# Kernel optimization log

Measured on AMD Instinct MI355X. Metric: run time of the kernel, lower is better.

Reference implementation:

```python
import jax, jax.numpy as jnp
import numpy as np

K = 20          # hard-coded self.k
NEG_SLOPE = 0.01


def _conv_bn_act(x, W, g, b):
    """1x1 conv (W: [Cout,Cin]) + eval-mode BN folded into per-channel g,b + LeakyReLU.
    x: (B, Cin, ...) -> (B, Cout, ...)"""
    y = jnp.einsum('oc,bc...->bo...', W, x)
    shp = (1, -1) + (1,) * (y.ndim - 2)
    return jax.nn.leaky_relu(y * g.reshape(shp) + b.reshape(shp), NEG_SLOPE)


def _knn_idx(x, k):
    """x: (B, C, N) -> idx (B, N, k) of k nearest neighbors (incl. self)."""
    xx = jnp.sum(x * x, axis=1)                      # (B, N)
    inner = jnp.einsum('bcn,bcm->bnm', x, x)         # (B, N, N)
    pair = 2.0 * inner - xx[:, :, None] - xx[:, None, :]  # -||xi-xj||^2
    return jax.lax.top_k(pair, k)[1]


def _gather(xt, idx):
    """xt: (B, N, C), idx: (B, N, k) -> (B, N, k, C)"""
    b = jnp.arange(xt.shape[0])[:, None, None]
    return xt[b, idx]


def _forward(x, w1, g1, b1, w2, g2, b2, wdg1, gdg1, bdg1, wdg2, gdg2, bdg2,
             wsn1, gsn1, bsn1, wsn2, gsn2, bsn2, w3, g3, b3, w4, g4, b4, w5, g5, b5):
    x0 = jnp.transpose(x, (0, 2, 1))                 # (B, 3, N) == xInit3d (t3d=False)
    h = _conv_bn_act(x0, w1, g1, b1)                 # (B, 64, N)
    h = _conv_bn_act(h, w2, g2, b2)                  # (B, 64, N)

    # Dynamic-graph EdgeConv: knn on features, edge = [x_i, x_j - x_i]
    idx1 = _knn_idx(h, K)                            # (B, N, K)
    ht = jnp.transpose(h, (0, 2, 1))                 # (B, N, 64)
    nbr = _gather(ht, idx1)                          # (B, N, K, 64)
    ctr = ht[:, :, None, :]                          # (B, N, 1, 64)
    edge = jnp.concatenate([jnp.broadcast_to(ctr, nbr.shape), nbr - ctr], axis=-1)
    edge = jnp.transpose(edge, (0, 3, 1, 2))         # (B, 128, N, K)
    h = _conv_bn_act(edge, wdg1, gdg1, bdg1)         # (B, 64, N, K)
    h = _conv_bn_act(h, wdg2, gdg2, bdg2)
    h = jnp.max(h, axis=-1)                          # (B, 64, N)

    # Spatial-neighborhood conv: knn on 3D coords, gather features only (cat=False)
    idx2 = _knn_idx(x0, K)                           # (B, N, K)
    feat2 = _gather(jnp.transpose(h, (0, 2, 1)), idx2)   # (B, N, K, 64)
    feat2 = jnp.transpose(feat2, (0, 3, 1, 2))       # (B, 64, N, K)
    h = _conv_bn_act(feat2, wsn1, gsn1, bsn1)
    h = _conv_bn_act(h, wsn2, gsn2, bsn2)
    h = jnp.max(h, axis=-1)                          # (B, 64, N)

    h = _conv_bn_act(h, w3, g3, b3)                  # (B, 64, N)
    h = _conv_bn_act(h, w4, g4, b4)                  # (B, 128, N)
    h = _conv_bn_act(h, w5, g5, b5)                  # (B, 512, N)
    return h[..., None]                             # (B, 512, N, 1)


def setup_inputs() -> dict:
    key = jax.random.key(0)
    ks = jax.random.split(key, 32)
    B, N = 8, 4096
    emb = 512
    d = {"x": jax.random.normal(ks[0], (B, N, 3), dtype=jnp.float32)}
    layers = [("1", 64, 3), ("2", 64, 64), ("dg1", 64, 128), ("dg2", 64, 64),
              ("sn1", 64, 64), ("sn2", 64, 64), ("3", 64, 64), ("4", 128, 64), ("5", emb, 128)]
    i = 1
    for name, co, ci in layers:
        d["w" + name] = jax.random.normal(ks[i], (co, ci), dtype=jnp.float32) * (1.0 / np.sqrt(ci))
        d["g" + name] = 1.0 + 0.1 * jax.random.normal(ks[i + 1], (co,), dtype=jnp.float32)
        d["b" + name] = 0.1 * jax.random.normal(ks[i + 2], (co,), dtype=jnp.float32)
        i += 3
    return d


def reference(x, w1, g1, b1, w2, g2, b2, wdg1, gdg1, bdg1, wdg2, gdg2, bdg2,
              wsn1, gsn1, bsn1, wsn2, gsn2, bsn2, w3, g3, b3, w4, g4, b4, w5, g5, b5):
    return _forward(x, w1, g1, b1, w2, g2, b2, wdg1, gdg1, bdg1, wdg2, gdg2, bdg2,
                    wsn1, gsn1, bsn1, wsn2, gsn2, bsn2, w3, g3, b3, w4, g4, b4, w5, g5, b5)
```

## Files before the change

kernel.cpp:

```cpp
#include <hip/hip_runtime.h>
#include <hip/hip_bf16.h>
#include <stdint.h>

typedef __hip_bfloat16 bf16;

#define N_   4096
#define NP   32768
#define KNN  20

#define OFF_H2   0L
#define OFF_XYZ  2097152L
#define OFF_X    2097152L
#define OFF_Y    2129920L
#define OFF_Z    2162688L
#define OFF_XX   2195456L
#define OFF_XXC  2228224L
#define OFF_IDX1 2260992L
#define OFF_P4   2260992L
#define OFF_IDX2 2916352L
#define OFF_WF   3571712L
#define OFF_FLAG 3676480L
#define OFF_PAIR 3676544L
#define OFF_U    3676544L
#define OFF_V    5773696L
#define OFF_HDG  7870848L
#define OFF_H4   5773696L

#define WF_W1 0
#define WF_G1 192
#define WF_B1 256
#define WF_W2 320
#define WF_G2 4416
#define WF_B2 4480
#define WF_WDG1 4544
#define WF_GDG1 12736
#define WF_BDG1 12800
#define WF_WDG2 12864
#define WF_GDG2 16960
#define WF_BDG2 17024
#define WF_WSN1 17088
#define WF_GSN1 21184
#define WF_BSN1 21248
#define WF_WSN2 21312
#define WF_GSN2 25408
#define WF_BSN2 25472
#define WF_W3 25536
#define WF_G3 29632
#define WF_B3 29696
#define WF_W4 29760
#define WF_G4 37952
#define WF_B4 38080
#define WF_W5 38208
#define WF_G5 103744
#define WF_B5 104256
#define WF_END 104768

__device__ __forceinline__ float lrelu(float x){ return x >= 0.f ? x : 0.01f*x; }

__device__ __forceinline__ float distf(float xn,float yn,float zn,
                                       float xm,float ym,float zm,float cm){
  return fmaf(2.f, fmaf(xn,xm, fmaf(yn,ym, zn*zm)), -cm);
}

template<int CTRL>
__device__ __forceinline__ float fmax_dpp(float v){
  int o = __builtin_amdgcn_update_dpp(0, __float_as_int(v), CTRL, 0xF, 0xF, true);
  return fmaxf(v, __int_as_float(o));
}
__device__ __forceinline__ float wave_max_bcast(float v){
  v = fmax_dpp<0xB1>(v);
  v = fmax_dpp<0x4E>(v);
  v = fmax_dpp<0x124>(v);
  v = fmax_dpp<0x128>(v);
  v = fmax_dpp<0x142>(v);
  v = fmax_dpp<0x143>(v);
  return __int_as_float(__builtin_amdgcn_readlane(__float_as_int(v), 63));
}

__device__ __forceinline__ void ins2(float c, int m, float& k1, int& i1,
                                     float& k2, int& i2){
  bool g1 = c > k1, g2 = c > k2;
  k2 = g2 ? (g1 ? k1 : c) : k2;
  i2 = g2 ? (g1 ? i1 : m) : i2;
  k1 = g1 ? c : k1;
  i1 = g1 ? m : i1;
}

template<int MODE, typename F>
__device__ __forceinline__ void topk_pairs(float k1, int i1, float k2, int i2,
                                           int lane, F&& refetch,
                                           int* __restrict__ outp){
  const float NEGINF = -__builtin_inff();
  uint32_t mlo = 0, mhi = 0;
  int keep = 0;
  #pragma unroll 1
  for (int tt = 0; tt < KNN; tt++){
    float g = wave_max_bcast(k1);
    uint64_t ball = __ballot(k1 == g);
    int js = __builtin_amdgcn_readfirstlane((int)(__ffsll((unsigned long long)ball) - 1));
    int wid = __builtin_amdgcn_readlane(i1, js);
    int kown = __builtin_amdgcn_readlane(__float_as_int(k2), js);
    if (lane == tt) keep = wid;
    bool own = (lane == js);
    uint32_t ord = (MODE == 0) ? ((uint32_t)wid >> 6)
                               : ((((uint32_t)wid >> 8) << 2) | ((uint32_t)wid & 3u));
    uint32_t blo = (ord < 32u) ? (1u << ord) : 0u;
    uint32_t bhi = (ord >= 32u) ? (1u << (ord - 32u)) : 0u;
    mlo |= own ? blo : 0u;
    mhi |= own ? bhi : 0u;
    k1 = own ? k2 : k1;  i1 = own ? i2 : i1;
    k2 = own ? NEGINF : k2;
    if (kown == (int)0xFF800000u){
      uint32_t mre = (MODE == 0)
        ? ((uint32_t)js + ((uint32_t)lane << 6))
        : ((((uint32_t)lane >> 2) << 8) | (((uint32_t)js) << 2) | ((uint32_t)lane & 3u));
      float v = refetch(mre);
      uint32_t bl = (uint32_t)__builtin_amdgcn_readlane((int)mlo, js);
      uint32_t bh = (uint32_t)__builtin_amdgcn_readlane((int)mhi, js);
      uint64_t bm = ((uint64_t)bh << 32) | bl;
      if ((bm >> lane) & 1ull) v = NEGINF;
      float g2 = wave_max_bcast(v);
      uint64_t b2 = __ballot(v == g2);
      int jw = (int)(__ffsll((unsigned long long)b2) - 1);
      uint32_t wm = (MODE == 0)
        ? ((uint32_t)js + ((uint32_t)jw << 6))
        : ((((uint32_t)jw >> 2) << 8) | (((uint32_t)js) << 2) | ((uint32_t)jw & 3u));
      if (lane == js){ k1 = g2; i1 = (int)wm; }
    }
  }
  if (lane < KNN) outp[lane] = keep;
}

__global__ void k_detect(const void* __restrict__ x, int* __restrict__ flag){
  int lane = threadIdx.x;
  const bf16* xb = (const bf16*)x;
  int cnt = 0;
  #pragma unroll 1
  for (int i = lane; i < 256; i += 64){
    float v = __bfloat162float(xb[2*i]);
    float a = fabsf(v);
    if (a > 1e-3f && a < 100.f) cnt++;
  }
  #pragma unroll
  for (int off = 32; off; off >>= 1) cnt += __shfl_down(cnt, off, 64);
  if (lane == 0) *flag = (cnt >= 128) ? 0 : 1;
}

struct WPack {
  const void* p[27];
  int off[28];
};

__global__ void k_wcvt(WPack pk, float* __restrict__ dst, const int* __restrict__ flagp){
  int i = blockIdx.x*256 + threadIdx.x;
  if (i >= WF_END) return;
  int f = *flagp;
  #pragma unroll 1
  for (int s = 0; s < 27; s++){
    if (i < pk.off[s+1]){
      int j = i - pk.off[s];
      dst[i] = f ? ((const float*)pk.p[s])[j]
                 : __bfloat162float(((const bf16*)pk.p[s])[j]);
      return;
    }
  }
}

__global__ void k_point(const void* __restrict__ x, float* __restrict__ ws){
  const float* wf = ws + OFF_WF;
  int f = ((const int*)(ws + OFF_FLAG))[0];
  int n = blockIdx.x*256 + threadIdx.x;
  float x0, x1, x2;
  if (f){
    const float* xf = (const float*)x;
    x0 = xf[n*3+0]; x1 = xf[n*3+1]; x2 = xf[n*3+2];
  } else {
    const bf16* xb = (const bf16*)x;
    x0 = __bfloat162float(xb[n*3+0]);
    x1 = __bfloat162float(xb[n*3+1]);
    x2 = __bfloat162float(xb[n*3+2]);
  }

  float h1[64];
  #pragma unroll
  for (int o=0;o<64;o++){
    float a = wf[WF_W1+o*3+0]*x0 + wf[WF_W1+o*3+1]*x1 + wf[WF_W1+o*3+2]*x2;
    h1[o] = lrelu(wf[WF_G1+o]*a + wf[WF_B1+o]);
  }
  float xx = 0.f;
  #pragma unroll 1
  for (int o=0;o<64;o++){
    float a = 0.f;
    #pragma unroll
    for (int c=0;c<64;c++) a += wf[WF_W2+o*64+c]*h1[c];
    float h2 = lrelu(wf[WF_G2+o]*a + wf[WF_B2+o]);
    ws[OFF_H2 + (long)n*64 + o] = h2;
    xx += h2*h2;
  }
  ws[OFF_XX + n] = xx;
  float cc = x0*x0 + x1*x1 + x2*x2;
  ws[OFF_X + n] = x0; ws[OFF_Y + n] = x1; ws[OFF_Z + n] = x2;
  ws[OFF_XXC + n] = cc;
  *(float4*)(ws + OFF_P4 + 4L*n) = make_float4(x0, x1, x2, cc);
}

__global__ __launch_bounds__(256) void k_pair(const float* __restrict__ ws, float* __restrict__ pair,
                                              int b, int n0){
  __shared__ float As[64*128];
  __shared__ float Bs[64*128];
  int t = threadIdx.x;
  int bx = blockIdx.x, by = blockIdx.y;
  const float* h2 = ws + OFF_H2 + (long)b*N_*64;

  int r = t >> 1, c0 = (t & 1)*32;
  const float4* arow = (const float4*)(h2 + (long)(n0 + by*128 + r)*64 + c0);
  const float4* brow = (const float4*)(h2 + (long)(bx*128 + r)*64 + c0);
  #pragma unroll
  for (int q=0;q<8;q++){
    float4 av = arow[q];
    As[(c0+4*q+0)*128 + r] = av.x; As[(c0+4*q+1)*128 + r] = av.y;
    As[(c0+4*q+2)*128 + r] = av.z; As[(c0+4*q+3)*128 + r] = av.w;
    float4 bv = brow[q];
    Bs[(c0+4*q+0)*128 + r] = bv.x; Bs[(c0+4*q+1)*128 + r] = bv.y;
    Bs[(c0+4*q+2)*128 + r] = bv.z; Bs[(c0+4*q+3)*128 + r] = bv.w;
  }
  __syncthreads();

  int tr = t/16, tc = t%16;
  float acc[8][8] = {};
  #pragma unroll 4
  for (int k=0;k<64;k++){
    const float4* ap = (const float4*)&As[k*128 + tr*8];
    const float4* bp = (const float4*)&Bs[k*128 + tc*8];
    float4 a0 = ap[0], a1 = ap[1], c0v = bp[0], c1v = bp[1];
    float a[8] = {a0.x,a0.y,a0.z,a0.w,a1.x,a1.y,a1.z,a1.w};
    float c[8] = {c0v.x,c0v.y,c0v.z,c0v.w,c1v.x,c1v.y,c1v.z,c1v.w};
    #pragma unroll
    for (int i=0;i<8;i++)
      #pragma unroll
      for (int j=0;j<8;j++) acc[i][j] += a[i]*c[j];
  }
  const float* xxp = ws + OFF_XX + b*N_ + bx*128 + tc*8;
  float xxm[8];
  #pragma unroll
  for (int j=0;j<8;j++) xxm[j] = xxp[j];
  #pragma unroll
  for (int i=0;i<8;i++){
    long row = (long)(by*128 + tr*8 + i)*N_ + bx*128 + tc*8;
    float4 o0 = make_float4(2.f*acc[i][0]-xxm[0], 2.f*acc[i][1]-xxm[1],
                            2.f*acc[i][2]-xxm[2], 2.f*acc[i][3]-xxm[3]);
    float4 o1 = make_float4(2.f*acc[i][4]-xxm[4], 2.f*acc[i][5]-xxm[5],
                            2.f*acc[i][6]-xxm[6], 2.f*acc[i][7]-xxm[7]);
    ((float4*)(pair+row))[0] = o0;
    ((float4*)(pair+row))[1] = o1;
  }
}

__global__ __launch_bounds__(256) void k_topk_pair(const float* __restrict__ pair, int* __restrict__ idx1,
                                                   int b, int n0){
  int t = threadIdx.x;
  int lane = t & 63, wv = t >> 6;
  int r = blockIdx.x*4 + wv;
  const float* rowp = pair + (long)r*N_;
  const float4* src = (const float4*)rowp;
  float k1 = -__builtin_inff(), k2 = -__builtin_inff();
  int i1 = 0, i2 = 0;
  #pragma unroll
  for (int q=0;q<16;q++){
    float4 v = src[lane + 64*q];
    int m0 = 4*lane + 256*q;
    ins2(v.x, m0,   k1,i1,k2,i2);
    ins2(v.y, m0+1, k1,i1,k2,i2);
    ins2(v.z, m0+2, k1,i1,k2,i2);
    ins2(v.w, m0+3, k1,i1,k2,i2);
  }
  topk_pairs<1>(k1,i1,k2,i2, lane, [&](uint32_t mre){ return rowp[mre]; },
                idx1 + (long)(b*N_ + n0 + r)*KNN);
}

__global__ __launch_bounds__(512) void k_knn2(const float* __restrict__ ws, int* __restrict__ idx2){
  __shared__ float4 pbuf[2][512];
  int t = threadIdx.x;
  int lane = t & 63, wv = t >> 6;
  int n = blockIdx.x*8 + wv;
  int base = n & ~4095;
  const float4* P4 = (const float4*)(ws + OFF_P4);
  float4 qp = P4[n];
  float xn = qp.x, yn = qp.y, zn = qp.z;
  float k1 = -__builtin_inff(), k2 = -__builtin_inff();
  int i1 = 0, i2 = 0;

  pbuf[0][t] = P4[base + t];
  __syncthreads();
  #pragma unroll 1
  for (int c = 0; c < 8; c++){
    float4 nx;
    if (c < 7) nx = P4[base + (c+1)*512 + t];
    const float4* pb = pbuf[c & 1];
    #pragma unroll
    for (int j = 0; j < 8; j++){
      float4 p = pb[lane + 64*j];
      int m = c*512 + 64*j + lane;
      ins2(distf(xn,yn,zn, p.x,p.y,p.z,p.w), m, k1,i1,k2,i2);
    }
    __syncthreads();
    if (c < 7) pbuf[(c+1) & 1][t] = nx;
    __syncthreads();
  }
  topk_pairs<0>(k1,i1,k2,i2, lane, [&](uint32_t mre){
      float4 p = P4[base + (int)mre];
      return distf(xn,yn,zn, p.x, p.y, p.z, p.w);
    }, idx2 + (long)n*KNN);
}

__global__ __launch_bounds__(256) void k_uv(float* __restrict__ ws){
  const float* wf = ws + OFF_WF;
  int t = threadIdx.x;
  int lane = t & 63;
  int W = blockIdx.x*4 + (t >> 6);
  int g = __builtin_amdgcn_readfirstlane(W >> 3);
  int s = __builtin_amdgcn_readfirstlane(W & 7);
  int n = g*64 + lane;
  int o0 = s*8;
  float h[64];
  const float4* src = (const float4*)(ws + OFF_H2 + (long)n*64);
  #pragma unroll
  for (int q=0;q<16;q++){ float4 v = src[q]; h[4*q]=v.x; h[4*q+1]=v.y; h[4*q+2]=v.z; h[4*q+3]=v.w; }
  float ua[8], vv[8];
  #pragma unroll 1
  for (int j=0;j<8;j++){
    int o = o0 + j;
    float va=0.f, vb=0.f;
    #pragma unroll
    for (int c=0;c<64;c++){
      va += wf[WF_WDG1+o*128+c]*h[c];
      vb += wf[WF_WDG1+o*128+64+c]*h[c];
    }
    ua[j] = va - vb;
    vv[j] = vb;
  }
  float* up = ws + OFF_U + (long)n*64 + o0;
  *(float4*)up     = make_float4(ua[0],ua[1],ua[2],ua[3]);
  *(float4*)(up+4) = make_float4(ua[4],ua[5],ua[6],ua[7]);
  float* vp = ws + OFF_V + (long)n*64 + o0;
  *(float4*)vp     = make_float4(vv[0],vv[1],vv[2],vv[3]);
  *(float4*)(vp+4) = make_float4(vv[4],vv[5],vv[6],vv[7]);
}

template<int USE_U>
__global__ __launch_bounds__(512) void k_edge(float* __restrict__ ws, const int* __restrict__ idxt,
      long uoff, long goff, int w2off,
      int g1off, int b1off, int g2off, int b2off, long outoff){
  __shared__ float y1t[64*66];
  __shared__ float w2t[64*68];
  __shared__ int   idxs[64*KNN];
  const float* wf = ws + OFF_WF;
  int t = threadIdx.x;
  int p0 = blockIdx.x*64;
  int b  = p0 >> 12;
  int lane = t & 63, wv = t >> 6;
  int tr = t & 31, oc = t >> 5;

  #pragma unroll 1
  for (int i=t;i<4096;i+=512){ int o = i>>6, kk = i&63; w2t[kk*68+o] = wf[w2off + i]; }
  #pragma unroll 1
  for (int i=t;i<64*KNN;i+=512) idxs[i] = idxt[(long)p0*KNN + i];

  float ur[8];
  if (USE_U){
    #pragma unroll
    for (int jj=0;jj<8;jj++)
      ur[jj] = ws[uoff + (long)(p0 + wv*8 + jj)*64 + lane];
  } else {
    #pragma unroll
    for (int jj=0;jj<8;jj++) ur[jj] = 0.f;
  }
  float g1v = wf[g1off+lane], b1v = wf[b1off+lane];
  float g2r[4], b2r[4];
  #pragma unroll
  for (int j=0;j<4;j++){ g2r[j] = wf[g2off+oc*4+j]; b2r[j] = wf[b2off+oc*4+j]; }

  float mx[2][4];
  #pragma unroll
  for (int i=0;i<2;i++)
    #pragma unroll
    for (int j=0;j<4;j++) mx[i][j] = -3.0e38f;

  __syncthreads();

  long gbase = goff + ((long)b << 12)*64;
  float pf[8];
  #pragma unroll
  for (int jj=0;jj<8;jj++){
    int nb = idxs[(wv*8 + jj)*KNN];
    pf[jj] = ws[gbase + (long)nb*64 + lane];
  }

  for (int k=0;k<KNN;k++){
    #pragma unroll
    for (int jj=0;jj<8;jj++){
      int e = wv*8 + jj;
      float val = pf[jj];
      if (USE_U) val += ur[jj];
      y1t[lane*66 + e] = lrelu(g1v*val + b1v);
    }
    __syncthreads();
    if (k+1 < KNN){
      #pragma unroll
      for (int jj=0;jj<8;jj++){
        int nb = idxs[(wv*8 + jj)*KNN + k+1];
        pf[jj] = ws[gbase + (long)nb*64 + lane];
      }
    }
    float acc[2][4] = {};
    #pragma unroll 4
    for (int kk=0;kk<64;kk++){
      float2 a = *(const float2*)&y1t[kk*66 + tr*2];
      float4 c = *(const float4*)&w2t[kk*68 + oc*4];
      float av[2] = {a.x, a.y};
      float cv[4] = {c.x, c.y, c.z, c.w};
      #pragma unroll
      for (int i=0;i<2;i++)
        #pragma unroll
        for (int j=0;j<4;j++) acc[i][j] += av[i]*cv[j];
    }
    #pragma unroll
    for (int i=0;i<2;i++)
      #pragma unroll
      for (int j=0;j<4;j++){
        float yy = lrelu(g2r[j]*acc[i][j] + b2r[j]);
        mx[i][j] = fmaxf(mx[i][j], yy);
      }
    __syncthreads();
  }
  #pragma unroll
  for (int i=0;i<2;i++)
    #pragma unroll
    for (int j=0;j<4;j++)
      ws[outoff + (long)(p0 + tr*2 + i)*64 + oc*4 + j] = mx[i][j];
}

__global__ __launch_bounds__(256) void k_w(float* __restrict__ ws){
  const float* wf = ws + OFF_WF;
  int t = threadIdx.x;
  int lane = t & 63;
  int W = blockIdx.x*4 + (t >> 6);
  int g = __builtin_amdgcn_readfirstlane(W >> 3);
  int s = __builtin_amdgcn_readfirstlane(W & 7);
  int n = g*64 + lane;
  int o0 = s*8;
  float h[64];
  const float4* src = (const float4*)(ws + OFF_HDG + (long)n*64);
  #pragma unroll
  for (int q=0;q<16;q++){ float4 v = src[q]; h[4*q]=v.x; h[4*q+1]=v.y; h[4*q+2]=v.z; h[4*q+3]=v.w; }
  float ua[8];
  #pragma unroll 1
  for (int j=0;j<8;j++){
    int o = o0 + j;
    float a = 0.f;
    #pragma unroll
    for (int c=0;c<64;c++) a += wf[WF_WSN1 + o*64 + c]*h[c];
    ua[j] = a;
  }
  float* up = ws + OFF_U + (long)n*64 + o0;
  *(float4*)up     = make_float4(ua[0],ua[1],ua[2],ua[3]);
  *(float4*)(up+4) = make_float4(ua[4],ua[5],ua[6],ua[7]);
}

__global__ __launch_bounds__(256) void k_h4(const float* __restrict__ ws, float* __restrict__ h4g){
  __shared__ float Hs[64*65];
  __shared__ float wb[64*130];
  const float* wf = ws + OFF_WF;
  int t = threadIdx.x;
  int p0 = blockIdx.x*64;

  {
    int r = t >> 2, c0 = (t & 3)*16;
    const float4* src = (const float4*)(ws + OFF_H2 + (long)(p0 + r)*64 + c0);
    #pragma unroll
    for (int q=0;q<4;q++){
      float4 v = src[q];
      Hs[(c0+4*q+0)*65 + r] = v.x; Hs[(c0+4*q+1)*65 + r] = v.y;
      Hs[(c0+4*q+2)*65 + r] = v.z; Hs[(c0+4*q+3)*65 + r] = v.w;
    }
  }
  {
    int r = t >> 2, c0 = (t & 3)*16;
    const float4* src = (const float4*)(wf + WF_W3 + (long)r*64 + c0);
    #pragma unroll
    for (int q=0;q<4;q++){
      float4 v = src[q];
      wb[(c0+4*q+0)*65 + r] = v.x; wb[(c0+4*q+1)*65 + r] = v.y;
      wb[(c0+4*q+2)*65 + r] = v.z; wb[(c0+4*q+3)*65 + r] = v.w;
    }
  }
  __syncthreads();

  int pr = t & 15, og = t >> 4;
  float acc[4][4] = {};
  #pragma unroll 8
  for (int k=0;k<64;k++){
    float4 a = *(const float4*)&Hs[k*65 + pr*4];
    float4 c = *(const float4*)&wb[k*65 + og*4];
    float av[4] = {a.x,a.y,a.z,a.w}, cv[4] = {c.x,c.y,c.z,c.w};
    #pragma unroll
    for (int i=0;i<4;i++)
      #pragma unroll
      for (int j=0;j<4;j++) acc[i][j] += av[i]*cv[j];
  }
  __syncthreads();

  #pragma unroll
  for (int j=0;j<4;j++){
    int o = og*4 + j;
    float g3 = wf[WF_G3+o], b3 = wf[WF_B3+o];
    #pragma unroll
    for (int i=0;i<4;i++)
      Hs[o*65 + pr*4 + i] = lrelu(g3*acc[i][j] + b3);
  }
  {
    int r = t >> 1, c0 = (t & 1)*32;
    const float4* src = (const float4*)(wf + WF_W4 + (long)r*64 + c0);
    #pragma unroll
    for (int q=0;q<8;q++){
      float4 v = src[q];
      wb[(c0+4*q+0)*130 + r] = v.x; wb[(c0+4*q+1)*130 + r] = v.y;
      wb[(c0+4*q+2)*130 + r] = v.z; wb[(c0+4*q+3)*130 + r] = v.w;
    }
  }
  __syncthreads();

  float a2[4][8] = {};
  #pragma unroll 8
  for (int k=0;k<64;k++){
    float4 a = *(const float4*)&Hs[k*65 + pr*4];
    float4 c0 = *(const float4*)&wb[k*130 + og*8];
    float4 c1 = *(const float4*)&wb[k*130 + og*8 + 4];
    float av[4] = {a.x,a.y,a.z,a.w};
    float cv[8] = {c0.x,c0.y,c0.z,c0.w,c1.x,c1.y,c1.z,c1.w};
    #pragma unroll
    for (int i=0;i<4;i++)
      #pragma unroll
      for (int j=0;j<8;j++) a2[i][j] += av[i]*cv[j];
  }
  #pragma unroll
  for (int j=0;j<8;j++){
    int o = og*8 + j;
    float g4 = wf[WF_G4+o], b4 = wf[WF_B4+o];
    #pragma unroll
    for (int i=0;i<4;i++)
      h4g[(long)o*NP + p0 + pr*4 + i] = lrelu(g4*a2[i][j] + b4);
  }
}

#define KC 32
__global__ __launch_bounds__(256) void k_conv5(const float* __restrict__ ws, void* __restrict__ outv){
  __shared__ float As[KC*128];
  __shared__ float Bs[KC*128];
  const float* wf = ws + OFF_WF;
  int f = ((const int*)(ws + OFF_FLAG))[0];
  int t = threadIdx.x;
  int p0 = blockIdx.x*128;
  int o0 = blockIdx.y*128;
  const float* H4 = ws + OFF_H4;
  float acc[8][8] = {};

  for (int kc = 0; kc < 128; kc += KC){
    {
      int r = t >> 1, c0 = (t & 1)*16;
      const float4* src = (const float4*)(wf + WF_W5 + (long)(o0 + r)*128 + kc + c0);
      #pragma unroll
      for (int q=0;q<4;q++){
        float4 v = src[q];
        As[(c0+4*q+0)*128 + r] = v.x; As[(c0+4*q+1)*128 + r] = v.y;
        As[(c0+4*q+2)*128 + r] = v.z; As[(c0+4*q+3)*128 + r] = v.w;
      }
    }
    {
      int kr = t >> 3, pc = (t & 7)*16;
      const float4* src = (const float4*)(H4 + (long)(kc + kr)*NP + p0 + pc);
      float4 v0 = src[0], v1 = src[1], v2 = src[2], v3 = src[3];
      *(float4*)&Bs[kr*128 + pc     ] = v0;
      *(float4*)&Bs[kr*128 + pc + 4 ] = v1;
      *(float4*)&Bs[kr*128 + pc + 8 ] = v2;
      *(float4*)&Bs[kr*128 + pc + 12] = v3;
    }
    __syncthreads();
    int tr = t/16, tc = t%16;
    #pragma unroll 8
    for (int k=0;k<KC;k++){
      const float4* ap = (const float4*)&As[k*128 + tr*8];
      const float4* bp = (const float4*)&Bs[k*128 + tc*8];
      float4 a0 = ap[0], a1 = ap[1], b0 = bp[0], b1 = bp[1];
      float a[8] = {a0.x,a0.y,a0.z,a0.w,a1.x,a1.y,a1.z,a1.w};
      float b[8] = {b0.x,b0.y,b0.z,b0.w,b1.x,b1.y,b1.z,b1.w};
      #pragma unroll
      for (int i=0;i<8;i++)
        #pragma unroll
        for (int j=0;j<8;j++) acc[i][j] += a[i]*b[j];
    }
    __syncthreads();
  }

  int tr = t/16, tc = t%16;
  int b = p0 >> 12, nn = (p0 & 4095) + tc*8;
  #pragma unroll
  for (int i=0;i<8;i++){
    int oo = o0 + tr*8 + i;
    float g5 = wf[WF_G5+oo], b5 = wf[WF_B5+oo];
    long base = ((long)(b*512 + oo) << 12) + nn;
    if (f){
      float4 v0 = make_float4(lrelu(g5*acc[i][0]+b5), lrelu(g5*acc[i][1]+b5),
                              lrelu(g5*acc[i][2]+b5), lrelu(g5*acc[i][3]+b5));
      float4 v1 = make_float4(lrelu(g5*acc[i][4]+b5), lrelu(g5*acc[i][5]+b5),
                              lrelu(g5*acc[i][6]+b5), lrelu(g5*acc[i][7]+b5));
      *(float4*)((float*)outv + base)     = v0;
      *(float4*)((float*)outv + base + 4) = v1;
    } else {
      #pragma unroll
      for (int j=0;j<8;j++)
        ((bf16*)outv)[base + j] = __float2bfloat16(lrelu(g5*acc[i][j] + b5));
    }
  }
}

extern "C" void kernel_launch(void* const* d_in, const int* in_sizes, int n_in,
                              void* d_out, int out_size, void* d_ws, size_t ws_size,
                              hipStream_t stream) {
  const void* X = d_in[0];
  float* ws = (float*)d_ws;
  int* flagp = (int*)(ws + OFF_FLAG);

  WPack pk;
  static const int wsz[27] = {192,64,64, 4096,64,64, 8192,64,64, 4096,64,64, 4096,64,64,
                              4096,64,64, 4096,64,64, 8192,128,128, 65536,512,512};
  int off = 0;
  for (int i=0;i<27;i++){ pk.p[i] = d_in[i+1]; pk.off[i] = off; off += wsz[i]; }
  pk.off[27] = off;

  k_detect<<<dim3(1), dim3(64), 0, stream>>>(X, flagp);
  k_wcvt<<<dim3((WF_END+255)/256), dim3(256), 0, stream>>>(pk, ws + OFF_WF, flagp);
  k_point<<<dim3(NP/256), dim3(256), 0, stream>>>(X, ws);
  k_knn2<<<dim3(NP/8), dim3(512), 0, stream>>>(ws, (int*)(ws + OFF_IDX2));

  long availf = (long)(ws_size/4) - OFF_PAIR;
  int chunk = 4096;
  if (availf < (long)N_*N_){
    long c = (availf / N_) & ~127L;
    chunk = (int)(c < 128 ? 128 : c);
    if (chunk > 4096) chunk = 4096;
  }
  for (int b=0;b<8;b++){
    for (int n0=0;n0<N_; n0+=chunk){
      int rows = (N_ - n0 < chunk) ? (N_ - n0) : chunk;
      k_pair<<<dim3(32, rows/128), dim3(256), 0, stream>>>(ws, ws + OFF_PAIR, b, n0);
      k_topk_pair<<<dim3(rows/4), dim3(256), 0, stream>>>(ws + OFF_PAIR, (int*)(ws + OFF_IDX1), b, n0);
    }
  }
  k_uv<<<dim3(NP/32), dim3(256), 0, stream>>>(ws);
  k_edge<1><<<dim3(NP/64), dim3(512), 0, stream>>>(ws, (const int*)(ws + OFF_IDX1),
        OFF_U, OFF_V, WF_WDG2, WF_GDG1, WF_BDG1, WF_GDG2, WF_BDG2, OFF_HDG);
  k_w<<<dim3(NP/32), dim3(256), 0, stream>>>(ws);
  k_edge<0><<<dim3(NP/64), dim3(512), 0, stream>>>(ws, (const int*)(ws + OFF_IDX2),
        0, OFF_U, WF_WSN2, WF_GSN1, WF_BSN1, WF_GSN2, WF_BSN2, OFF_H2);
  k_h4<<<dim3(NP/64), dim3(256), 0, stream>>>(ws, ws + OFF_H4);
  k_conv5<<<dim3(NP/128, 4), dim3(256), 0, stream>>>(ws, d_out);
}
```

Before: 1.028 ms.

## Process two neighbors per edge iteration and read pre-transposed W2 from global

A small kernel writes transposed copies of the two second-layer edge weights into a free workspace region. The edge kernel reads them as float4 from global/cache instead of staging them in shared memory. The neighbor loop now handles two neighbors per iteration with double y1 buffers, so each weight load is reused across both and barriers are halved. The cost is more registers per thread and global-memory weight reads inside the inner loop.

```diff
diff --git a/kernel.cpp b/kernel.cpp
--- a/kernel.cpp
+++ b/kernel.cpp
@@ -14,6 +14,7 @@
 #define OFF_Y    2129920L
 #define OFF_Z    2162688L
 #define OFF_XX   2195456L
+#define OFF_W2T  2195456L
 #define OFF_XXC  2228224L
 #define OFF_IDX1 2260992L
 #define OFF_P4   2260992L
@@ -166,6 +167,18 @@
   }
 }
 
+__global__ void k_wt(float* __restrict__ ws){
+  const float* wf = ws + OFF_WF;
+  int src = blockIdx.x ? WF_WSN2 : WF_WDG2;
+  long dst = OFF_W2T + (long)blockIdx.x*4096;
+  int t = threadIdx.x;
+  #pragma unroll
+  for (int i=t;i<4096;i+=256){
+    int o = i >> 6, kk = i & 63;
+    ws[dst + (long)kk*64 + o] = wf[src + o*64 + kk];
+  }
+}
+
 __global__ void k_point(const void* __restrict__ x, float* __restrict__ ws){
   const float* wf = ws + OFF_WF;
   int f = ((const int*)(ws + OFF_FLAG))[0];
@@ -349,12 +362,13 @@
 
 template<int USE_U>
 __global__ __launch_bounds__(512) void k_edge(float* __restrict__ ws, const int* __restrict__ idxt,
-      long uoff, long goff, int w2off,
+      long uoff, long goff, long w2toff,
       int g1off, int b1off, int g2off, int b2off, long outoff){
-  __shared__ float y1t[64*66];
-  __shared__ float w2t[64*68];
+  __shared__ float y1a[64*66];
+  __shared__ float y1b[64*66];
   __shared__ int   idxs[64*KNN];
   const float* wf = ws + OFF_WF;
+  const float4* w2t = (const float4*)(ws + w2toff);
   int t = threadIdx.x;
   int p0 = blockIdx.x*64;
   int b  = p0 >> 12;
@@ -362,8 +376,6 @@
   int tr = t & 31, oc = t >> 5;
 
   #pragma unroll 1
-  for (int i=t;i<4096;i+=512){ int o = i>>6, kk = i&63; w2t[kk*68+o] = wf[w2off + i]; }
-  #pragma unroll 1
   for (int i=t;i<64*KNN;i+=512) idxs[i] = idxt[(long)p0*KNN + i];
 
   float ur[8];
@@ -389,47 +401,56 @@
   __syncthreads();
 
   long gbase = goff + ((long)b << 12)*64;
-  float pf[8];
+  float pfa[8], pfb[8];
   #pragma unroll
   for (int jj=0;jj<8;jj++){
-    int nb = idxs[(wv*8 + jj)*KNN];
-    pf[jj] = ws[gbase + (long)nb*64 + lane];
-  }
-
-  for (int k=0;k<KNN;k++){
+    int e = wv*8 + jj;
+    pfa[jj] = ws[gbase + (long)idxs[e*KNN + 0]*64 + lane];
+    pfb[jj] = ws[gbase + (long)idxs[e*KNN + 1]*64 + lane];
+  }
+
+  for (int c=0;c<KNN/2;c++){
     #pragma unroll
     for (int jj=0;jj<8;jj++){
       int e = wv*8 + jj;
-      float val = pf[jj];
-      if (USE_U) val += ur[jj];
-      y1t[lane*66 + e] = lrelu(g1v*val + b1v);
+      float va = pfa[jj];
+      float vb = pfb[jj];
+      if (USE_U){ va += ur[jj]; vb += ur[jj]; }
+      y1a[lane*66 + e] = lrelu(g1v*va + b1v);
+      y1b[lane*66 + e] = lrelu(g1v*vb + b1v);
     }
     __syncthreads();
-    if (k+1 < KNN){
+    if (c+1 < KNN/2){
       #pragma unroll
       for (int jj=0;jj<8;jj++){
-        int nb = idxs[(wv*8 + jj)*KNN + k+1];
-        pf[jj] = ws[gbase + (long)nb*64 + lane];
+        int e = wv*8 + jj;
+        pfa[jj] = ws[gbase + (long)idxs[e*KNN + 2*c+2]*64 + lane];
+        pfb[jj] = ws[gbase + (long)idxs[e*KNN + 2*c+3]*64 + lane];
       }
     }
-    float acc[2][4] = {};
+    float acca[2][4] = {}, accb[2][4] = {};
     #pragma unroll 4
     for (int kk=0;kk<64;kk++){
-      float2 a = *(const float2*)&y1t[kk*66 + tr*2];
-      float4 c = *(const float4*)&w2t[kk*68 + oc*4];
+      float2 a  = *(const float2*)&y1a[kk*66 + tr*2];
+      float2 bb = *(const float2*)&y1b[kk*66 + tr*2];
+      float4 cv = w2t[kk*16 + oc];
       float av[2] = {a.x, a.y};
-      float cv[4] = {c.x, c.y, c.z, c.w};
+      float bv[2] = {bb.x, bb.y};
+      float cvv[4] = {cv.x, cv.y, cv.z, cv.w};
       #pragma unroll
       for (int i=0;i<2;i++)
         #pragma unroll
-        for (int j=0;j<4;j++) acc[i][j] += av[i]*cv[j];
+        for (int j=0;j<4;j++){
+          acca[i][j] += av[i]*cvv[j];
+          accb[i][j] += bv[i]*cvv[j];
+        }
     }
     #pragma unroll
     for (int i=0;i<2;i++)
       #pragma unroll
       for (int j=0;j<4;j++){
-        float yy = lrelu(g2r[j]*acc[i][j] + b2r[j]);
-        mx[i][j] = fmaxf(mx[i][j], yy);
+        mx[i][j] = fmaxf(mx[i][j], lrelu(g2r[j]*acca[i][j] + b2r[j]));
+        mx[i][j] = fmaxf(mx[i][j], lrelu(g2r[j]*accb[i][j] + b2r[j]));
       }
     __syncthreads();
   }
@@ -657,12 +678,13 @@
       k_topk_pair<<<dim3(rows/4), dim3(256), 0, stream>>>(ws + OFF_PAIR, (int*)(ws + OFF_IDX1), b, n0);
     }
   }
+  k_wt<<<dim3(2), dim3(256), 0, stream>>>(ws);
   k_uv<<<dim3(NP/32), dim3(256), 0, stream>>>(ws);
   k_edge<1><<<dim3(NP/64), dim3(512), 0, stream>>>(ws, (const int*)(ws + OFF_IDX1),
-        OFF_U, OFF_V, WF_WDG2, WF_GDG1, WF_BDG1, WF_GDG2, WF_BDG2, OFF_HDG);
+        OFF_U, OFF_V, OFF_W2T, WF_GDG1, WF_BDG1, WF_GDG2, WF_BDG2, OFF_HDG);
   k_w<<<dim3(NP/32), dim3(256), 0, stream>>>(ws);
   k_edge<0><<<dim3(NP/64), dim3(512), 0, stream>>>(ws, (const int*)(ws + OFF_IDX2),
-        0, OFF_U, WF_WSN2, WF_GSN1, WF_BSN1, WF_GSN2, WF_BSN2, OFF_H2);
+        0, OFF_U, OFF_W2T + 4096, WF_GSN1, WF_BSN1, WF_GSN2, WF_BSN2, OFF_H2);
   k_h4<<<dim3(NP/64), dim3(256), 0, stream>>>(ws, ws + OFF_H4);
   k_conv5<<<dim3(NP/128, 4), dim3(256), 0, stream>>>(ws, d_out);
 }
```

New measurement: 1.023 ms. No clear change (-0.5%).
